# Kernel optimization log

Measured on AMD Instinct MI355X. Metric: run time of the kernel, lower is better.

## Reference

```python
import jax, jax.numpy as jnp
import numpy as np
import math

B_, S_, D_ = 8, 2048, 512
N_ = 16
EXPAND = 1.5
INNER = math.ceil(D_ * EXPAND)  # 768
K_ = 3
DELTA_MIN = 1e-4
DELTA_MAX = 3.0


def _hippo(n):
    A = np.zeros((n, n), np.float32)
    for i in range(n):
        ci = math.sqrt(2 * i + 1)
        for m in range(i + 1):
            cm = math.sqrt(2 * m + 1)
            if i == m:
                A[i, m] = -(2 * i + 1)
            else:
                A[i, m] = (-1.0 if (i - m) % 2 == 0 else 1.0) * ci * cm
    idx = np.arange(n, dtype=np.float32)
    Bv = np.sqrt(2.0 * idx + 1.0)
    Cv = Bv.copy()
    Cv[1::2] *= -1.0
    return A, Bv, Cv


def setup_inputs() -> dict:
    key = jax.random.key(0)
    k0, k1, k2, k3 = jax.random.split(key, 4)
    A0, Bv, Cv = _hippo(N_)
    scale = 1.0 / math.sqrt(INNER)
    return {
        "x": jax.random.normal(k0, (B_, S_, D_), jnp.float32),
        "ln_g": jnp.ones((D_,), jnp.float32),
        "ln_b": jnp.zeros((D_,), jnp.float32),
        "W_in": jax.random.normal(k1, (3 * INNER, D_), jnp.float32) / math.sqrt(D_),
        "conv_w": jax.random.normal(k2, (INNER, 1, K_), jnp.float32) / math.sqrt(K_),
        "A": jnp.asarray(A0),
        "Bmat": jnp.asarray(np.repeat(Bv[:, None], INNER, axis=1) * scale),  # (N, inner)
        "Cmat": jnp.asarray(np.repeat(Cv[None, :], INNER, axis=0) * scale),  # (inner, N)
        "W_out": jax.random.normal(k3, (D_, INNER), jnp.float32) / math.sqrt(INNER),
    }


def reference(x, ln_g, ln_b, W_in, conv_w, A, Bmat, Cmat, W_out):
    B, S, D = x.shape
    N = A.shape[0]
    # LayerNorm
    mu = jnp.mean(x, -1, keepdims=True)
    var = jnp.var(x, -1, keepdims=True)
    h = (x - mu) / jnp.sqrt(var + 1e-5) * ln_g + ln_b
    # Input projection -> data / gate / delta_raw
    proj = h @ W_in.T  # (B,S,3*inner)
    inner = proj.shape[-1] // 3
    data, gate, delta_raw = jnp.split(proj, 3, axis=-1)
    # Depthwise conv with padding K-1 then truncation to S == causal left pad K-1
    K = conv_w.shape[-1]
    dc = jax.lax.conv_general_dilated(
        data.transpose(0, 2, 1), conv_w, window_strides=(1,),
        padding=[(K - 1, 0)], dimension_numbers=("NCH", "OIH", "NCH"),
        feature_group_count=inner,
    ).transpose(0, 2, 1)  # (B,S,inner)
    u = jax.nn.silu(dc)
    # Data-dependent step size
    delta = jnp.mean(jax.nn.softplus(delta_raw), -1, keepdims=True) + DELTA_MIN
    delta = jnp.minimum(delta, DELTA_MAX)  # (B,S,1)
    # ZOH discretisation: A_disc = expm(delta*A); B_disc = A^{-1}(A_disc - I) B
    scaled_A = delta[..., None] * A  # (B,S,N,N)
    A_disc = jax.vmap(jax.scipy.linalg.expm)(scaled_A.reshape(-1, N, N)).reshape(B, S, N, N)
    rhs = A_disc - jnp.eye(N, dtype=x.dtype)
    integral = jnp.linalg.solve(jnp.broadcast_to(A, rhs.shape), rhs)  # (B,S,N,N)
    B_disc = integral @ Bmat  # (B,S,N,inner)

    def step(state, inputs):  # state: (B,N)
        Ad, Bd, ut = inputs  # (B,N,N), (B,N,inner), (B,inner)
        state = jnp.einsum("bnm,bm->bn", Ad, state) + jnp.einsum("bnd,bd->bn", Bd, ut)
        y = jnp.einsum("dn,bn->bd", Cmat, state)  # (B,inner)
        return state, y

    s0 = jnp.zeros((B, N), x.dtype)
    _, ys = jax.lax.scan(
        step, s0,
        (A_disc.transpose(1, 0, 2, 3), B_disc.transpose(1, 0, 2, 3), u.transpose(1, 0, 2)),
    )
    selective = ys.transpose(1, 0, 2)  # (B,S,inner)
    out = (jax.nn.sigmoid(gate) * selective) @ W_out.T
    return x + out
```

## Files before the change

kernel.cpp:

```cpp
#include <hip/hip_runtime.h>
#include <hip/hip_bf16.h>
#include <math.h>

#define BB 8
#define SS 2048
#define DD 512
#define II 768
#define MT (BB*SS)
#define NS 16
#define CH 32
#define NCB (SS/CH)
#define NCHK (MT/CH)
#define NT 1024

typedef __hip_bfloat16 bf16;
typedef __attribute__((ext_vector_type(8))) short bf16x8;
typedef __attribute__((ext_vector_type(4))) float f32x4;

__device__ __forceinline__ float fsigm(float x){
  return __builtin_amdgcn_rcpf(1.f + __expf(-x));
}
__device__ __forceinline__ float fsoftp(float x){
  return (x > 15.f) ? x : __logf(1.f + __expf(x));
}
__device__ __forceinline__ unsigned short f2bf_bits(float f){
  __hip_bfloat16 h = __float2bfloat16(f);
  return __builtin_bit_cast(unsigned short, h);
}
__device__ __forceinline__ float bfbits2f(short s){
  union { float f; unsigned u; } v;
  v.u = ((unsigned)(unsigned short)s) << 16;
  return v.f;
}
__device__ __forceinline__ void gload16(const bf16* src, void* dst){
  __builtin_amdgcn_global_load_lds((const __attribute__((address_space(1))) void*)src,
                                   (__attribute__((address_space(3))) void*)dst, 16, 0, 0);
}
__device__ __forceinline__ void gload16f(const float* src, void* dst){
  __builtin_amdgcn_global_load_lds((const __attribute__((address_space(1))) void*)src,
                                   (__attribute__((address_space(3))) void*)dst, 16, 0, 0);
}
template<int KDIM>
__device__ __forceinline__ bf16x8 lds_a_frag(const bf16* As, int row, int kseg){
  return *(const bf16x8*)((const char*)As + (size_t)row*(KDIM*2)
                          + (size_t)((kseg ^ (row & 7)) << 4));
}

__global__ __launch_bounds__(256) void cast_kernel(
    const float* __restrict__ in, bf16* __restrict__ out, int n4)
{
  int i = blockIdx.x*256 + threadIdx.x;
  if (i >= n4) return;
  float4 v = *(const float4*)&in[(size_t)i*4];
  ushort4 o = make_ushort4(f2bf_bits(v.x), f2bf_bits(v.y), f2bf_bits(v.z), f2bf_bits(v.w));
  *(ushort4*)&out[(size_t)i*4] = o;
}

__global__ __launch_bounds__(256) void bmsplit_kernel(
    const float* __restrict__ Bm, bf16* __restrict__ hi, bf16* __restrict__ lo)
{
  int i = blockIdx.x*256 + threadIdx.x;
  if (i >= NS*II) return;
  float f = Bm[i];
  unsigned short hb = f2bf_bits(f);
  hi[i] = __builtin_bit_cast(bf16, hb);
  lo[i] = __float2bfloat16(f - bfbits2f((short)hb));
}

__global__ __launch_bounds__(256) void apow_kernel(
    const float* __restrict__ A, float* __restrict__ Apow)
{
  __shared__ double Am[256], T0[256], T1[256];
  __shared__ double colsum[16];
  int tid = threadIdx.x, r = tid>>4, c = tid&15;
  double a = (double)A[tid];
  Am[tid] = a; T0[tid] = a;
  Apow[tid] = A[tid];
  __syncthreads();
  double *Tc = T0, *Tn = T1;
  for (int k=2;k<=13;k++){
    double s = 0.0;
    #pragma unroll
    for (int j=0;j<16;j++) s += Tc[r*16+j]*Am[j*16+c];
    Tn[tid] = s;
    Apow[(k-1)*256 + tid] = (float)s;
    __syncthreads();
    double* tmp = Tc; Tc = Tn; Tn = tmp;
  }
  if (tid < 16){
    double s = 0.0;
    #pragma unroll
    for (int j=0;j<16;j++) s += fabs(Am[j*16+tid]);
    colsum[tid] = s;
  }
  __syncthreads();
  if (tid == 0){
    double mx = 0.0;
    #pragma unroll
    for (int j=0;j<16;j++) mx = fmax(mx, colsum[j]);
    Apow[13*256] = (float)mx;
  }
}

__global__ __launch_bounds__(64) void etab_kernel(
    const float* __restrict__ Apow, float* __restrict__ Etab,
    float* __restrict__ Gtab, float* __restrict__ dEtab)
{
  int i = blockIdx.x;
  int l = threadIdx.x;
  int r = l&15, gq = l>>4, c0 = gq*4;
  __shared__ alignas(16) float bufE[256];
  __shared__ alignas(16) float bufG[256];
  float delta = (3.0f*i)/(float)(NT-1);
  float anorm = Apow[13*256];
  float mx = delta*anorm;
  int s = 0;
  if (mx > 2.f){
    s = (int)ceilf(log2f(mx)) - 1;
    if (s < 0) s = 0;
    if (s > 12) s = 12;
  }
  float dsc = ldexpf(delta, -s);
  const float invk[14]  = {0.f, 1.f, 0.5f, 1.f/3.f, 0.25f, 0.2f, 1.f/6.f, 1.f/7.f,
                           0.125f, 1.f/9.f, 0.1f, 1.f/11.f, 1.f/12.f, 1.f/13.f};
  float4 e = make_float4(0.f,0.f,0.f,0.f), g = e;
  if (r==c0  ){ e.x = 1.f; g.x = dsc; }
  if (r==c0+1){ e.y = 1.f; g.y = dsc; }
  if (r==c0+2){ e.z = 1.f; g.z = dsc; }
  if (r==c0+3){ e.w = 1.f; g.w = dsc; }
  float ck = 1.f;
  #pragma unroll
  for (int k=1;k<=13;k++){
    ck *= dsc * invk[k];
    float gk = ck * dsc / (float)(k+1);
    float4 ap = *(const float4*)&Apow[(k-1)*256 + r*16 + c0];
    e.x = fmaf(ck, ap.x, e.x); e.y = fmaf(ck, ap.y, e.y);
    e.z = fmaf(ck, ap.z, e.z); e.w = fmaf(ck, ap.w, e.w);
    g.x = fmaf(gk, ap.x, g.x); g.y = fmaf(gk, ap.y, g.y);
    g.z = fmaf(gk, ap.z, g.z); g.w = fmaf(gk, ap.w, g.w);
  }
  for (int it=0; it<s; ++it){
    *(float4*)&bufE[r*16+c0] = e;
    *(float4*)&bufG[r*16+c0] = g;
    __syncthreads();
    float erow[16];
    #pragma unroll
    for (int q4=0;q4<4;q4++){
      float4 tv = *(const float4*)&bufE[r*16+q4*4];
      erow[q4*4+0]=tv.x; erow[q4*4+1]=tv.y; erow[q4*4+2]=tv.z; erow[q4*4+3]=tv.w;
    }
    float4 en = make_float4(0.f,0.f,0.f,0.f);
    float4 gn = g;
    #pragma unroll
    for (int kk=0;kk<16;kk++){
      float4 ev = *(const float4*)&bufE[kk*16+c0];
      float4 gv = *(const float4*)&bufG[kk*16+c0];
      float ek = erow[kk];
      en.x=fmaf(ek,ev.x,en.x); en.y=fmaf(ek,ev.y,en.y);
      en.z=fmaf(ek,ev.z,en.z); en.w=fmaf(ek,ev.w,en.w);
      gn.x=fmaf(ek,gv.x,gn.x); gn.y=fmaf(ek,gv.y,gn.y);
      gn.z=fmaf(ek,gv.z,gn.z); gn.w=fmaf(ek,gv.w,gn.w);
    }
    e = en; g = gn;
    __syncthreads();
  }
  size_t o = (size_t)i*256 + r*16 + c0;
  *(float4*)&Etab[o] = e;
  *(float4*)&Gtab[o] = g;
  *(float4*)&bufE[r*16+c0] = e;
  __syncthreads();
  float4 de = make_float4(0.f,0.f,0.f,0.f);
  #pragma unroll
  for (int q4=0;q4<4;q4++){
    float4 ar = *(const float4*)&Apow[r*16 + q4*4];
    float4 e0 = *(const float4*)&bufE[(q4*4+0)*16 + c0];
    float4 e1 = *(const float4*)&bufE[(q4*4+1)*16 + c0];
    float4 e2 = *(const float4*)&bufE[(q4*4+2)*16 + c0];
    float4 e3 = *(const float4*)&bufE[(q4*4+3)*16 + c0];
    de.x = fmaf(ar.x,e0.x,fmaf(ar.y,e1.x,fmaf(ar.z,e2.x,fmaf(ar.w,e3.x,de.x))));
    de.y = fmaf(ar.x,e0.y,fmaf(ar.y,e1.y,fmaf(ar.z,e2.y,fmaf(ar.w,e3.y,de.y))));
    de.z = fmaf(ar.x,e0.z,fmaf(ar.y,e1.z,fmaf(ar.z,e2.z,fmaf(ar.w,e3.z,de.z))));
    de.w = fmaf(ar.x,e0.w,fmaf(ar.y,e1.w,fmaf(ar.z,e2.w,fmaf(ar.w,e3.w,de.w))));
  }
  *(float4*)&dEtab[o] = de;
}

__global__ __launch_bounds__(256) void ln_kernel(
    const float* __restrict__ x, const float* __restrict__ g,
    const float* __restrict__ b, bf16* __restrict__ h)
{
  int w = threadIdx.x >> 6, l = threadIdx.x & 63;
  int m = blockIdx.x*4 + w;
  const float* xr = x + (size_t)m*DD;
  float4 v0 = *(const float4*)&xr[l*4];
  float4 v1 = *(const float4*)&xr[256 + l*4];
  float s  = v0.x+v0.y+v0.z+v0.w + v1.x+v1.y+v1.z+v1.w;
  float sq = v0.x*v0.x+v0.y*v0.y+v0.z*v0.z+v0.w*v0.w
           + v1.x*v1.x+v1.y*v1.y+v1.z*v1.z+v1.w*v1.w;
  #pragma unroll
  for (int o=1;o<64;o<<=1){ s += __shfl_xor(s,o); sq += __shfl_xor(sq,o); }
  float mu  = s*(1.f/DD);
  float var = sq*(1.f/DD) - mu*mu;
  float rs  = rsqrtf(var + 1e-5f);
  float4 g0 = *(const float4*)&g[l*4];
  float4 b0 = *(const float4*)&b[l*4];
  float4 g1 = *(const float4*)&g[256 + l*4];
  float4 b1 = *(const float4*)&b[256 + l*4];
  ushort4 o0, o1;
  o0.x = f2bf_bits((v0.x-mu)*rs*g0.x + b0.x);
  o0.y = f2bf_bits((v0.y-mu)*rs*g0.y + b0.y);
  o0.z = f2bf_bits((v0.z-mu)*rs*g0.z + b0.z);
  o0.w = f2bf_bits((v0.w-mu)*rs*g0.w + b0.w);
  o1.x = f2bf_bits((v1.x-mu)*rs*g1.x + b1.x);
  o1.y = f2bf_bits((v1.y-mu)*rs*g1.y + b1.y);
  o1.z = f2bf_bits((v1.z-mu)*rs*g1.z + b1.z);
  o1.w = f2bf_bits((v1.w-mu)*rs*g1.w + b1.w);
  *(ushort4*)&h[(size_t)m*DD + l*4]       = o0;
  *(ushort4*)&h[(size_t)m*DD + 256 + l*4] = o1;
}


__global__ __launch_bounds__(256, 3) void gemm1_mfma(
    const bf16* __restrict__ Ah, const bf16* __restrict__ Bw,
    bf16* __restrict__ databf, bf16* __restrict__ gatebf, float* __restrict__ dacc)
{
  __shared__ alignas(16) bf16 As[128*64];
  __shared__ alignas(16) bf16 Bs[128*64];
  const int tid = threadIdx.x, l = tid & 63, w = tid >> 6;
  const int lrow = l & 15, lgrp = l >> 4;
  const int orig = blockIdx.x;
  const int swz = (orig & 7) * (2304/8) + (orig >> 3);
  const int bm = (swz / 18) * 128;
  const int bn = swz % 18;
  const int wrow = (w >> 1) * 64, wcol = (w & 1) * 64;

  f32x4 acc[4][4];
  #pragma unroll
  for (int i=0;i<4;i++){
    #pragma unroll
    for (int f=0;f<4;f++){ f32x4 z={0.f,0.f,0.f,0.f}; acc[i][f]=z; }
  }

  for (int t=0; t<8; ++t){
    #pragma unroll
    for (int it=0; it<4; ++it){
      int d = tid + it*256;
      int r = d >> 3, s = d & 7;
      gload16(Ah + (size_t)(bm + r)*DD + t*64 + ((s ^ (r&7))<<3),
              (char*)As + (size_t)(d - l)*16);
    }
    #pragma unroll
    for (int it=0; it<4; ++it){
      int d = tid + it*256;
      int r = d >> 3, s = d & 7;
      gload16(Bw + (size_t)(bn*128 + r)*DD + t*64 + ((s ^ (r&7))<<3),
              (char*)Bs + (size_t)(d - l)*16);
    }
    __syncthreads();
    #pragma unroll
    for (int kk=0; kk<2; ++kk){
      bf16x8 afr[4], bfr[4];
      #pragma unroll
      for (int i=0;i<4;i++) afr[i] = lds_a_frag<64>(As, wrow + i*16 + lrow, kk*4 + lgrp);
      #pragma unroll
      for (int f=0;f<4;f++) bfr[f] = lds_a_frag<64>(Bs, wcol + f*16 + lrow, kk*4 + lgrp);
      #pragma unroll
      for (int i=0;i<4;i++){
        #pragma unroll
        for (int f=0;f<4;f++)
          acc[i][f] = __builtin_amdgcn_mfma_f32_16x16x32_bf16(afr[i], bfr[f], acc[i][f], 0,0,0);
      }
    }
    __syncthreads();
  }

  const int rowb = bm + wrow + lgrp*4;
  const int cglob = bn*128 + wcol + lrow;
  if (bn < 6){
    #pragma unroll
    for (int i=0;i<4;i++){
      #pragma unroll
      for (int f=0;f<4;f++){
        int col = cglob + f*16;
        #pragma unroll
        for (int j=0;j<4;j++)
          databf[(size_t)(rowb + i*16 + j)*II + col] = __float2bfloat16(acc[i][f][j]);
      }
    }
  } else if (bn < 12){
    #pragma unroll
    for (int i=0;i<4;i++){
      #pragma unroll
      for (int f=0;f<4;f++){
        int col = cglob - 768 + f*16;
        #pragma unroll
        for (int j=0;j<4;j++)
          gatebf[(size_t)(rowb + i*16 + j)*II + col] = __float2bfloat16(fsigm(acc[i][f][j]));
      }
    }
  } else {
    #pragma unroll
    for (int i=0;i<4;i++){
      #pragma unroll
      for (int j=0;j<4;j++){
        float v = fsoftp(acc[i][0][j]) + fsoftp(acc[i][1][j])
                + fsoftp(acc[i][2][j]) + fsoftp(acc[i][3][j]);
        v += __shfl_xor(v,1); v += __shfl_xor(v,2);
        v += __shfl_xor(v,4); v += __shfl_xor(v,8);
        if (lrow == 0) atomicAdd(&dacc[rowb + i*16 + j], v);
      }
    }
  }
}

__global__ __launch_bounds__(256, 3) void gemm2_mfma(
    const bf16* __restrict__ Asel, const bf16* __restrict__ Bw,
    const float* __restrict__ x, float* __restrict__ out)
{
  __shared__ alignas(16) bf16 As[128*64];
  __shared__ alignas(16) bf16 Bs[128*64];
  const int tid = threadIdx.x, l = tid & 63, w = tid >> 6;
  const int lrow = l & 15, lgrp = l >> 4;
  const int orig = blockIdx.x;
  const int swz = (orig & 7) * (512/8) + (orig >> 3);
  const int bm = (swz >> 2) * 128;
  const int bn = swz & 3;
  const int wrow = (w >> 1) * 64, wcol = (w & 1) * 64;

  f32x4 acc[4][4];
  #pragma unroll
  for (int i=0;i<4;i++){
    #pragma unroll
    for (int f=0;f<4;f++){ f32x4 z={0.f,0.f,0.f,0.f}; acc[i][f]=z; }
  }

  for (int t=0; t<12; ++t){
    #pragma unroll
    for (int it=0; it<4; ++it){
      int d = tid + it*256;
      int r = d >> 3, s = d & 7;
      gload16(Asel + (size_t)(bm + r)*II + t*64 + ((s ^ (r&7))<<3),
              (char*)As + (size_t)(d - l)*16);
    }
    #pragma unroll
    for (int it=0; it<4; ++it){
      int d = tid + it*256;
      int r = d >> 3, s = d & 7;
      gload16(Bw + (size_t)(bn*128 + r)*II + t*64 + ((s ^ (r&7))<<3),
              (char*)Bs + (size_t)(d - l)*16);
    }
    __syncthreads();
    #pragma unroll
    for (int kk=0; kk<2; ++kk){
      bf16x8 afr[4], bfr[4];
      #pragma unroll
      for (int i=0;i<4;i++) afr[i] = lds_a_frag<64>(As, wrow + i*16 + lrow, kk*4 + lgrp);
      #pragma unroll
      for (int f=0;f<4;f++) bfr[f] = lds_a_frag<64>(Bs, wcol + f*16 + lrow, kk*4 + lgrp);
      #pragma unroll
      for (int i=0;i<4;i++){
        #pragma unroll
        for (int f=0;f<4;f++)
          acc[i][f] = __builtin_amdgcn_mfma_f32_16x16x32_bf16(afr[i], bfr[f], acc[i][f], 0,0,0);
      }
    }
    __syncthreads();
  }

  const int rowb = bm + wrow + lgrp*4;
  #pragma unroll
  for (int i=0;i<4;i++){
    #pragma unroll
    for (int f=0;f<4;f++){
      int col = bn*128 + wcol + f*16 + lrow;
      #pragma unroll
      for (int j=0;j<4;j++){
        size_t e = (size_t)(rowb + i*16 + j)*DD + col;
        out[e] = acc[i][f][j] + x[e];
      }
    }
  }
}

__global__ __launch_bounds__(256) void convw_mfma(
    const bf16* __restrict__ data, const float* __restrict__ cw,
    const bf16* __restrict__ Bmhi, const bf16* __restrict__ Bmlo,
    float* __restrict__ w_all)
{
  __shared__ alignas(16) bf16  Ds[1728*8];
  __shared__ alignas(16) float cwl[II*3];
  __shared__ alignas(16) float red[4][256];
  const int tid = threadIdx.x, l = tid & 63, wv = tid >> 6;
  const int lrow = l & 15, lgrp = l >> 4;
  const int p0 = blockIdx.x * 16;
  const int p  = p0 + lrow;
  const int t  = p & (SS-1);
  const int bstart = p0 & ~(SS-1);
  const float mask1 = (t>=1) ? 1.f : 0.f;
  const float mask0 = (t>=2) ? 1.f : 0.f;

  #pragma unroll
  for (int it=0; it<7; ++it){
    int d = tid + it*256;
    if (d < 1728){
      int r = d % 18, s2 = d / 18;
      int prow = p0 - 2 + r; if (prow < bstart) prow = bstart;
      gload16(data + (size_t)prow*II + s2*8, (char*)Ds + (size_t)(d - l)*16);
    }
  }
  #pragma unroll
  for (int it=0; it<3; ++it){
    int d = tid + it*256;
    if (d < 576)
      gload16f(cw + d*4, (char*)cwl + (size_t)(d - l)*16);
  }
  __syncthreads();

  const int sB = wv*24 + lgrp;
  const char* DsB = (const char*)Ds + ((size_t)sB*18 + lrow)*16;
  const bf16* bh  = Bmhi + (size_t)lrow*II + sB*8;
  const bf16* bl  = Bmlo + (size_t)lrow*II + sB*8;
  const float* cwp = cwl + sB*24;

  f32x4 acc = {0.f,0.f,0.f,0.f};
  #pragma unroll
  for (int u=0; u<6; ++u){
    bf16x8 v0 = *(const bf16x8*)(DsB + (size_t)u*72*16);
    bf16x8 v1 = *(const bf16x8*)(DsB + (size_t)u*72*16 + 16);
    bf16x8 v2 = *(const bf16x8*)(DsB + (size_t)u*72*16 + 32);
    bf16x8 ah = *(const bf16x8*)(bh + u*32);
    bf16x8 al = *(const bf16x8*)(bl + u*32);
    float cv[24];
    #pragma unroll
    for (int q=0;q<6;q++){
      float4 cq = *(const float4*)(cwp + u*96 + q*4);
      cv[q*4+0]=cq.x; cv[q*4+1]=cq.y; cv[q*4+2]=cq.z; cv[q*4+3]=cq.w;
    }
    bf16x8 Bh, Bl;
    #pragma unroll
    for (int j=0;j<8;j++){
      float d2 = bfbits2f(v2[j]);
      float d1 = bfbits2f(v1[j]) * mask1;
      float d0 = bfbits2f(v0[j]) * mask0;
      float a = fmaf(d0, cv[3*j], fmaf(d1, cv[3*j+1], d2*cv[3*j+2]));
      float u2 = a * fsigm(a);
      unsigned short hb = f2bf_bits(u2);
      Bh[j] = (short)hb;
      Bl[j] = (short)f2bf_bits(u2 - bfbits2f((short)hb));
    }
    acc = __builtin_amdgcn_mfma_f32_16x16x32_bf16(ah, Bh, acc, 0,0,0);
    acc = __builtin_amdgcn_mfma_f32_16x16x32_bf16(ah, Bl, acc, 0,0,0);
    acc = __builtin_amdgcn_mfma_f32_16x16x32_bf16(al, Bh, acc, 0,0,0);
  }
  *(f32x4*)&red[wv][l*4] = acc;
  __syncthreads();
  if (wv == 0){
    f32x4 s0 = *(const f32x4*)&red[0][l*4];
    f32x4 s1 = *(const f32x4*)&red[1][l*4];
    f32x4 s2 = *(const f32x4*)&red[2][l*4];
    f32x4 s3 = *(const f32x4*)&red[3][l*4];
    f32x4 s = s0 + s1 + s2 + s3;
    *(f32x4*)&w_all[(size_t)p*NS + lgrp*4] = s;
  }
}

__global__ __launch_bounds__(256) void scan1_kernel(
    const float* __restrict__ Etab, const float* __restrict__ Gtab,
    const float* __restrict__ dEtab, const float* __restrict__ dacc,
    const float* __restrict__ w_all,
    float* __restrict__ c_all, float* __restrict__ P, float* __restrict__ q)
{
  int cc = blockIdx.x;
  int bb = cc / NCB, ci = cc % NCB;
  size_t base = (size_t)bb*SS + (size_t)ci*CH;
  int tid = threadIdx.x;
  int i = tid>>4, j = tid&15;
  __shared__ float Et[CH][256];
  __shared__ float cb[CH][16];
  __shared__ float Pb[2][256];
  __shared__ float qb[2][16];
  Pb[0][tid] = (i==j)?1.f:0.f;
  if (tid<16) qb[0][tid]=0.f;
  const float hh = 3.f/(float)(NT-1);
  for (int t=0;t<CH;t++){
    size_t m = base + t;
    float delta = fminf(dacc[m]*(1.f/II) + 1e-4f, 3.0f);
    float tf = delta * (float)(NT-1) * (1.f/3.f);
    int i0 = (int)tf;
    if (i0 > NT-2) i0 = NT-2;
    float fr = tf - (float)i0;
    float fr2 = fr*fr, fr3 = fr2*fr;
    float h00 = 2.f*fr3 - 3.f*fr2 + 1.f;
    float h10 = fr3 - 2.f*fr2 + fr;
    float h01 = -2.f*fr3 + 3.f*fr2;
    float h11 = fr3 - fr2;
    size_t o0 = (size_t)i0*256 + tid;
    float E0 = Etab[o0], E1 = Etab[o0+256];
    float D0 = dEtab[o0], D1 = dEtab[o0+256];
    float G0 = Gtab[o0], G1 = Gtab[o0+256];
    float e = h00*E0 + h01*E1 + hh*(h10*D0 + h11*D1);
    float g = h00*G0 + h01*G1 + hh*(h10*E0 + h11*E1);
    Et[t][j*16 + i] = e;
    float cv = g * w_all[m*NS + j];
    cv += __shfl_xor(cv,1); cv += __shfl_xor(cv,2);
    cv += __shfl_xor(cv,4); cv += __shfl_xor(cv,8);
    if (j==0){ c_all[m*NS + i] = cv; cb[t][i] = cv; }
  }
  __syncthreads();
  int cur = 0;
  for (int t=0;t<CH;t++){
    float acc2 = 0.f;
    #pragma unroll
    for (int k=0;k<16;k++) acc2 = fmaf(Et[t][k*16+i], Pb[cur][k*16+j], acc2);
    float qa = 0.f;
    if (j==0){
      #pragma unroll
      for (int k=0;k<16;k++) qa = fmaf(Et[t][k*16+i], qb[cur][k], qa);
      qa += cb[t][i];
    }
    Pb[cur^1][tid] = acc2;
    if (j==0) qb[cur^1][i] = qa;
    __syncthreads();
    cur ^= 1;
  }
  P[(size_t)cc*256 + tid] = Pb[cur][tid];
  if (tid<16) q[(size_t)cc*NS + tid] = qb[cur][tid];
}

__global__ __launch_bounds__(64) void scan2_kernel(
    const float* __restrict__ P, const float* __restrict__ q,
    float* __restrict__ entry)
{
  int b = blockIdx.x;
  int l = threadIdx.x;
  __shared__ alignas(16) float Pl[2][256];
  __shared__ float el[2][16];
  if (l < 16) el[0][l] = 0.f;
  gload16f(P + (size_t)(b*NCB)*256 + l*4, (char*)Pl[0]);
  float qv = q[(size_t)(b*NCB)*NS + (l & 15)];
  int cur = 0;
  for (int ci=0; ci<NCB; ci++){
    __syncthreads();
    int cc = b*NCB + ci;
    if (ci+1 < NCB)
      gload16f(P + (size_t)(cc+1)*256 + l*4, (char*)Pl[cur^1]);
    float qn = (ci+1 < NCB) ? q[(size_t)(cc+1)*NS + (l&15)] : 0.f;
    if (l < 16){
      entry[(size_t)cc*NS + l] = el[cur][l];
      float a = qv;
      #pragma unroll
      for (int k=0;k<16;k++) a = fmaf(Pl[cur][l*16+k], el[cur][k], a);
      el[cur^1][l] = a;
    }
    qv = qn;
    cur ^= 1;
  }
}

__global__ __launch_bounds__(256) void scan3sel_kernel(
    const float* __restrict__ Etab, const float* __restrict__ dEtab,
    const float* __restrict__ dacc, const float* __restrict__ c_all,
    const float* __restrict__ entry, const float* __restrict__ Cm,
    const bf16* __restrict__ gate, bf16* __restrict__ selg)
{
  __shared__ alignas(16) float Ads[CH*256];
  __shared__ alignas(16) float cl[CH*16];
  int cc = blockIdx.x;
  int bb = cc / NCB, ci = cc % NCB;
  size_t base = (size_t)bb*SS + (size_t)ci*CH;
  int tid = threadIdx.x, l = tid & 63, w = tid >> 6;
  int r = l & 15;
  int i = tid >> 4, j = tid & 15;
  if (tid < 128)
    gload16f(c_all + base*NS + tid*4, (char*)cl + (size_t)(tid - l)*16);

  float cmr[3][16];
  #pragma unroll
  for (int p=0;p<3;p++){
    int jcol = w*192 + p*64 + l;
    #pragma unroll
    for (int q4=0;q4<4;q4++){
      float4 cv = *(const float4*)&Cm[jcol*16 + q4*4];
      cmr[p][q4*4+0]=cv.x; cmr[p][q4*4+1]=cv.y;
      cmr[p][q4*4+2]=cv.z; cmr[p][q4*4+3]=cv.w;
    }
  }

  const float hh = 3.f/(float)(NT-1);
  const int wslot = (j>>2) ^ ((i>>1)&3);
  const int woff  = i*16 + wslot*4 + (j&3);
  for (int t=0;t<CH;t++){
    size_t m = base + t;
    float delta = fminf(dacc[m]*(1.f/II) + 1e-4f, 3.0f);
    float tf = delta * (float)(NT-1) * (1.f/3.f);
    int i0 = (int)tf;
    if (i0 > NT-2) i0 = NT-2;
    float fr = tf - (float)i0;
    float fr2 = fr*fr, fr3 = fr2*fr;
    float h00 = 2.f*fr3 - 3.f*fr2 + 1.f;
    float h10 = fr3 - 2.f*fr2 + fr;
    float h01 = -2.f*fr3 + 3.f*fr2;
    float h11 = fr3 - fr2;
    size_t o0 = (size_t)i0*256 + tid;
    float E0 = Etab[o0], E1 = Etab[o0+256];
    float D0 = dEtab[o0], D1 = dEtab[o0+256];
    Ads[t*256 + woff] = h00*E0 + h01*E1 + hh*(h10*D0 + h11*D1);
  }
  float g[16];
  #pragma unroll
  for (int k=0;k<16;k++) g[k] = entry[(size_t)cc*NS + k];
  __syncthreads();

  const int frm = (r>>1)&3;
  for (int t=0;t<CH;t++){
    size_t m = base + t;
    float s = cl[t*16 + r];
    #pragma unroll
    for (int q4=0;q4<4;q4++){
      float4 ev = *(const float4*)&Ads[(t*64 + r*4 + (q4 ^ frm))*4];
      s = fmaf(ev.x, g[q4*4+0], s);
      s = fmaf(ev.y, g[q4*4+1], s);
      s = fmaf(ev.z, g[q4*4+2], s);
      s = fmaf(ev.w, g[q4*4+3], s);
    }
    #pragma unroll
    for (int k=0;k<16;k++) g[k] = __shfl(s, k);
    #pragma unroll
    for (int p=0;p<3;p++){
      int jcol = w*192 + p*64 + l;
      float y = 0.f;
      #pragma unroll
      for (int k=0;k<16;k++) y = fmaf(cmr[p][k], g[k], y);
      size_t e = m*II + jcol;
      float gv = __bfloat162float(gate[e]);
      selg[e] = __float2bfloat16(gv*y);
    }
  }
}

extern "C" void kernel_launch(void* const* d_in, const int* in_sizes, int n_in,
                              void* d_out, int out_size, void* d_ws, size_t ws_size,
                              hipStream_t stream) {
  (void)in_sizes; (void)n_in; (void)out_size; (void)ws_size;
  const float* x      = (const float*)d_in[0];
  const float* ln_g   = (const float*)d_in[1];
  const float* ln_b   = (const float*)d_in[2];
  const float* W_in   = (const float*)d_in[3];
  const float* conv_w = (const float*)d_in[4];
  const float* A      = (const float*)d_in[5];
  const float* Bm     = (const float*)d_in[6];
  const float* Cm     = (const float*)d_in[7];
  const float* Wout   = (const float*)d_in[8];
  float* out = (float*)d_out;

  char* ws = (char*)d_ws;
  size_t off = 0;
  #define WSALLOC(ty, name, count) \
    ty* name = (ty*)(ws + off); off += (((size_t)(count))*sizeof(ty) + 255) & ~(size_t)255;
  WSALLOC(bf16,  hbf,    (size_t)MT*DD)
  WSALLOC(bf16,  databf, (size_t)MT*II)
  WSALLOC(bf16,  gatebf, (size_t)MT*II)
  WSALLOC(float, dacc,   MT)
  WSALLOC(float, w_all,  (size_t)MT*NS)
  WSALLOC(float, c_all,  (size_t)MT*NS)
  WSALLOC(float, Pbuf,   (size_t)NCHK*256)
  WSALLOC(float, qbuf,   (size_t)NCHK*NS)
  WSALLOC(float, entry,  (size_t)NCHK*NS)
  WSALLOC(bf16,  Winbf,  (size_t)3*II*DD)
  WSALLOC(bf16,  Woutbf, (size_t)DD*II)
  WSALLOC(bf16,  Bmhi,   (size_t)NS*II)
  WSALLOC(bf16,  Bmlo,   (size_t)NS*II)
  WSALLOC(float, Apow,   13*256 + 16)
  WSALLOC(float, Etab,   (size_t)NT*256)
  WSALLOC(float, Gtab,   (size_t)NT*256)
  WSALLOC(float, dEtab,  (size_t)NT*256)
  #undef WSALLOC

  hipMemsetAsync(dacc, 0, (size_t)MT*sizeof(float), stream);
  cast_kernel  <<<(3*II*DD/4 + 255)/256, 256, 0, stream>>>(W_in,  Winbf,  3*II*DD/4);
  cast_kernel  <<<(DD*II/4   + 255)/256, 256, 0, stream>>>(Wout,  Woutbf, DD*II/4);
  bmsplit_kernel<<<(NS*II + 255)/256, 256, 0, stream>>>(Bm, Bmhi, Bmlo);
  apow_kernel  <<<1, 256, 0, stream>>>(A, Apow);
  etab_kernel  <<<NT, 64, 0, stream>>>(Apow, Etab, Gtab, dEtab);
  ln_kernel    <<<MT/4, 256, 0, stream>>>(x, ln_g, ln_b, hbf);
  gemm1_mfma   <<<dim3(2304), 256, 0, stream>>>(hbf, Winbf, databf, gatebf, dacc);
  convw_mfma   <<<MT/16, 256, 0, stream>>>(databf, conv_w, Bmhi, Bmlo, w_all);
  scan1_kernel <<<NCHK, 256, 0, stream>>>(Etab, Gtab, dEtab, dacc, w_all, c_all, Pbuf, qbuf);
  scan2_kernel <<<BB, 64, 0, stream>>>(Pbuf, qbuf, entry);
  scan3sel_kernel<<<NCHK, 256, 0, stream>>>(Etab, dEtab, dacc, c_all, entry, Cm, gatebf, databf);
  gemm2_mfma   <<<dim3(512), 256, 0, stream>>>(databf, Woutbf, x, out);
}
```

Measured before the change: 207.9 us.

## Restructure gemm1 into 256x256 tiles with 4-stage async LDS pipeline

The input-projection GEMM moves from 128x128 tiles with 256 threads and a load/sync/compute loop to 256x256 tiles with 512 threads, K-step 32, and a 4-slot ring of LDS buffers filled three stages ahead using global_load_lds and explicit vmcnt waits. This is meant to hide global memory latency behind MFMA work and to raise arithmetic intensity per block. In exchange it uses much more LDS and more accumulator registers per wave (8x4 tiles), which may lower occupancy. The grid also shrinks to 576 blocks, which can cause wave-quantization imbalance across CUs. The delta-reduction epilogue still sums only four column fragments per wave, and each wave now covers 64 columns.

New measurement: 226.4 us. 1.09x slower.

```diff
diff --git a/kernel.cpp b/kernel.cpp
--- a/kernel.cpp
+++ b/kernel.cpp
@@ -44,6 +44,10 @@
 __device__ __forceinline__ bf16x8 lds_a_frag(const bf16* As, int row, int kseg){
   return *(const bf16x8*)((const char*)As + (size_t)row*(KDIM*2)
                           + (size_t)((kseg ^ (row & 7)) << 4));
+}
+__device__ __forceinline__ bf16x8 lds_frag32(const bf16* base, int row, int lg){
+  return *(const bf16x8*)((const char*)base + (size_t)row*64
+                          + (size_t)((lg ^ ((row>>1)&3)) << 4));
 }
 
 __global__ __launch_bounds__(256) void cast_kernel(
@@ -219,80 +223,89 @@
   *(ushort4*)&h[(size_t)m*DD + 256 + l*4] = o1;
 }
 
-
-__global__ __launch_bounds__(256, 3) void gemm1_mfma(
+__global__ __launch_bounds__(512, 2) void gemm1_mfma(
     const bf16* __restrict__ Ah, const bf16* __restrict__ Bw,
     bf16* __restrict__ databf, bf16* __restrict__ gatebf, float* __restrict__ dacc)
 {
-  __shared__ alignas(16) bf16 As[128*64];
-  __shared__ alignas(16) bf16 Bs[128*64];
-  const int tid = threadIdx.x, l = tid & 63, w = tid >> 6;
+  __shared__ alignas(16) bf16 AS[4][256*32];
+  __shared__ alignas(16) bf16 BS[4][256*32];
+  const int tid = threadIdx.x, l = tid & 63, wid = tid >> 6;
   const int lrow = l & 15, lgrp = l >> 4;
+  const int wm = wid >> 2, wn = wid & 3;
   const int orig = blockIdx.x;
-  const int swz = (orig & 7) * (2304/8) + (orig >> 3);
-  const int bm = (swz / 18) * 128;
-  const int bn = swz % 18;
-  const int wrow = (w >> 1) * 64, wcol = (w & 1) * 64;
-
-  f32x4 acc[4][4];
-  #pragma unroll
-  for (int i=0;i<4;i++){
+  const int swz = (orig & 7) * (576/8) + (orig >> 3);
+  const int bm = (swz / 9) * 256;
+  const int bn = swz % 9;
+
+  f32x4 acc[8][4];
+  #pragma unroll
+  for (int i=0;i<8;i++){
     #pragma unroll
     for (int f=0;f<4;f++){ f32x4 z={0.f,0.f,0.f,0.f}; acc[i][f]=z; }
   }
 
-  for (int t=0; t<8; ++t){
-    #pragma unroll
-    for (int it=0; it<4; ++it){
-      int d = tid + it*256;
-      int r = d >> 3, s = d & 7;
-      gload16(Ah + (size_t)(bm + r)*DD + t*64 + ((s ^ (r&7))<<3),
-              (char*)As + (size_t)(d - l)*16);
-    }
-    #pragma unroll
-    for (int it=0; it<4; ++it){
-      int d = tid + it*256;
-      int r = d >> 3, s = d & 7;
-      gload16(Bw + (size_t)(bn*128 + r)*DD + t*64 + ((s ^ (r&7))<<3),
-              (char*)Bs + (size_t)(d - l)*16);
-    }
-    __syncthreads();
-    #pragma unroll
-    for (int kk=0; kk<2; ++kk){
-      bf16x8 afr[4], bfr[4];
-      #pragma unroll
-      for (int i=0;i<4;i++) afr[i] = lds_a_frag<64>(As, wrow + i*16 + lrow, kk*4 + lgrp);
-      #pragma unroll
-      for (int f=0;f<4;f++) bfr[f] = lds_a_frag<64>(Bs, wcol + f*16 + lrow, kk*4 + lgrp);
-      #pragma unroll
-      for (int i=0;i<4;i++){
-        #pragma unroll
-        for (int f=0;f<4;f++)
-          acc[i][f] = __builtin_amdgcn_mfma_f32_16x16x32_bf16(afr[i], bfr[f], acc[i][f], 0,0,0);
-      }
-    }
-    __syncthreads();
-  }
-
-  const int rowb = bm + wrow + lgrp*4;
-  const int cglob = bn*128 + wcol + lrow;
-  if (bn < 6){
-    #pragma unroll
-    for (int i=0;i<4;i++){
+  auto stage = [&](int X){
+    const int slot = X & 3;
+    #pragma unroll
+    for (int it=0; it<2; ++it){
+      int d = tid + it*512;
+      int r = d >> 2, s = d & 3;
+      gload16(Ah + (size_t)(bm + r)*DD + X*32 + ((s ^ ((r>>1)&3))<<3),
+              (char*)AS[slot] + (size_t)(d - l)*16);
+    }
+    #pragma unroll
+    for (int it=0; it<2; ++it){
+      int d = tid + it*512;
+      int r = d >> 2, s = d & 3;
+      gload16(Bw + (size_t)(bn*256 + r)*DD + X*32 + ((s ^ ((r>>1)&3))<<3),
+              (char*)BS[slot] + (size_t)(d - l)*16);
+    }
+  };
+
+  stage(0); stage(1); stage(2);
+
+  #pragma unroll 1
+  for (int X=0; X<16; ++X){
+    if (X < 14)      asm volatile("s_waitcnt vmcnt(8)" ::: "memory");
+    else if (X == 14) asm volatile("s_waitcnt vmcnt(4)" ::: "memory");
+    else              asm volatile("s_waitcnt vmcnt(0)" ::: "memory");
+    __builtin_amdgcn_s_barrier();
+    asm volatile("" ::: "memory");
+    if (X <= 12) stage(X+3);
+    const bf16* Ab = AS[X & 3];
+    const bf16* Bb = BS[X & 3];
+    bf16x8 af[8], bfr[4];
+    #pragma unroll
+    for (int i=0;i<8;i++) af[i] = lds_frag32(Ab, wm*128 + i*16 + lrow, lgrp);
+    #pragma unroll
+    for (int f=0;f<4;f++) bfr[f] = lds_frag32(Bb, wn*64 + f*16 + lrow, lgrp);
+    #pragma unroll
+    for (int i=0;i<8;i++){
+      #pragma unroll
+      for (int f=0;f<4;f++)
+        acc[i][f] = __builtin_amdgcn_mfma_f32_16x16x32_bf16(af[i], bfr[f], acc[i][f], 0,0,0);
+    }
+  }
+
+  const int rowb = bm + wm*128 + lgrp*4;
+  const int cbase = bn*256 + wn*64 + lrow;
+  if (bn < 3){
+    #pragma unroll
+    for (int i=0;i<8;i++){
       #pragma unroll
       for (int f=0;f<4;f++){
-        int col = cglob + f*16;
+        int col = cbase + f*16;
         #pragma unroll
         for (int j=0;j<4;j++)
           databf[(size_t)(rowb + i*16 + j)*II + col] = __float2bfloat16(acc[i][f][j]);
       }
     }
-  } else if (bn < 12){
-    #pragma unroll
-    for (int i=0;i<4;i++){
+  } else if (bn < 6){
+    #pragma unroll
+    for (int i=0;i<8;i++){
       #pragma unroll
       for (int f=0;f<4;f++){
-        int col = cglob - 768 + f*16;
+        int col = cbase - 768 + f*16;
         #pragma unroll
         for (int j=0;j<4;j++)
           gatebf[(size_t)(rowb + i*16 + j)*II + col] = __float2bfloat16(fsigm(acc[i][f][j]));
@@ -300,7 +313,7 @@
     }
   } else {
     #pragma unroll
-    for (int i=0;i<4;i++){
+    for (int i=0;i<8;i++){
       #pragma unroll
       for (int j=0;j<4;j++){
         float v = fsoftp(acc[i][0][j]) + fsoftp(acc[i][1][j])
@@ -683,7 +696,7 @@
   apow_kernel  <<<1, 256, 0, stream>>>(A, Apow);
   etab_kernel  <<<NT, 64, 0, stream>>>(Apow, Etab, Gtab, dEtab);
   ln_kernel    <<<MT/4, 256, 0, stream>>>(x, ln_g, ln_b, hbf);
-  gemm1_mfma   <<<dim3(2304), 256, 0, stream>>>(hbf, Winbf, databf, gatebf, dacc);
+  gemm1_mfma   <<<dim3(576), 512, 0, stream>>>(hbf, Winbf, databf, gatebf, dacc);
   convw_mfma   <<<MT/16, 256, 0, stream>>>(databf, conv_w, Bmhi, Bmlo, w_all);
   scan1_kernel <<<NCHK, 256, 0, stream>>>(Etab, Gtab, dEtab, dacc, w_all, c_all, Pbuf, qbuf);
   scan2_kernel <<<BB, 64, 0, stream>>>(Pbuf, qbuf, entry);
```
